# Optimization experiments

Measured on AMD Instinct MI355X. Metric: run time of the kernel, lower is better.

## Reference

```python
import jax, jax.numpy as jnp
import numpy as np

B, C, H, W = 16, 512, 64, 64
NH, HD = 8, 64  # num_heads, head_dim; C == NH*HD
EPS_ATTN = 1e-5
EPS_BN = 1e-5


def setup_inputs() -> dict:
    key = jax.random.key(0)
    k = jax.random.split(key, 9)
    x = jax.random.normal(k[0], (B, C, H, W), dtype=jnp.float32)
    # grouped 1x1 conv qkv: groups=NH, in/group=HD, out/group=3*HD
    w1 = jax.random.normal(k[1], (NH, 3 * HD, HD), dtype=jnp.float32) * 0.05
    b1 = jax.random.normal(k[2], (NH, 3 * HD), dtype=jnp.float32) * 0.01
    # grouped 1x1 conv qkv2: groups=HD, in/group=NH, out/group=3*NH
    w2 = jax.random.normal(k[3], (HD, 3 * NH, NH), dtype=jnp.float32) * 0.05
    b2 = jax.random.normal(k[4], (HD, 3 * NH), dtype=jnp.float32) * 0.01
    gamma = 1.0 + 0.1 * jax.random.normal(k[5], (C,), dtype=jnp.float32)
    beta = 0.1 * jax.random.normal(k[6], (C,), dtype=jnp.float32)
    rmean = 0.1 * jax.random.normal(k[7], (C,), dtype=jnp.float32)
    rvar = 0.5 + jax.random.uniform(k[8], (C,), dtype=jnp.float32)
    return {"x": x, "w1": w1, "b1": b1, "w2": w2, "b2": b2,
            "gamma": gamma, "beta": beta, "rmean": rmean, "rvar": rvar}


def _signed_sqrt_softmax(a):
    a = jnp.sign(a) * jnp.sqrt(jnp.abs(a) + EPS_ATTN)
    return jax.nn.softmax(a, axis=-1)


def reference(x, w1, b1, w2, b2, gamma, beta, rmean, rvar):
    N = H * W
    # ---- stage 1: grouped 1x1 conv (groups=NH) ----
    xg = x.reshape(B, NH, HD, N)
    qkv = jnp.einsum('goi,bgin->bgon', w1, xg) + b1[None, :, :, None]  # [B,NH,3HD,N]
    # torch grouped-conv channel order is group-major -> flatten then split as in source
    q, k, v = jnp.moveaxis(qkv.reshape(B, 3 * C, N).reshape(B, 3, NH, HD, N), 1, 0)
    attn = jnp.einsum('bhdn,bhen->bhde', q, k) * (HD ** -0.5)  # [B,NH,HD,HD]
    attn = _signed_sqrt_softmax(attn)
    out = jnp.einsum('bhde,bhen->bhdn', attn, v)  # [B,NH,HD,N]
    x1 = out.reshape(B, C, H, W) + x
    x1 = jnp.transpose(x1.reshape(B, NH, HD, H, W), (0, 2, 1, 3, 4)).reshape(B, C, H, W)
    # ---- BatchNorm2d (eval mode) + ReLU ----
    inv = gamma / jnp.sqrt(rvar + EPS_BN)
    y = x1 * inv[None, :, None, None] + (beta - rmean * inv)[None, :, None, None]
    xr = jnp.maximum(y, 0.0)
    # ---- stage 2: grouped 1x1 conv (groups=HD) ----
    xg2 = xr.reshape(B, HD, NH, N)
    qkv2 = jnp.einsum('goi,bgin->bgon', w2, xg2) + b2[None, :, :, None]  # [B,HD,3NH,N]
    q2, k2, v2 = jnp.moveaxis(qkv2.reshape(B, 3 * C, N).reshape(B, 3, HD, NH, N), 1, 0)
    attn2 = jnp.einsum('bdhn,bden->bdhe', q2, k2) * (NH ** -0.5)  # [B,HD,NH,NH]
    attn2 = _signed_sqrt_softmax(attn2)
    out2 = jnp.einsum('bdhe,bden->bdhn', attn2, v2)  # [B,HD,NH,N]
    x2 = jnp.transpose(out2.reshape(B, HD, NH, H, W), (0, 2, 1, 3, 4)).reshape(B, C, H, W) + y
    return x2
```

## Files before the change

kernel.cpp:

```cpp
#include <hip/hip_runtime.h>

#define N_ 4096

typedef __attribute__((ext_vector_type(8))) short bf16x8;
typedef __attribute__((ext_vector_type(4))) short bf16x4;
typedef __attribute__((ext_vector_type(4))) float f32x4;

__device__ __forceinline__ float ssqrt(float a) {
  if (a == 0.f) return 0.f;
  return copysignf(sqrtf(fabsf(a) + 1e-5f), a);
}

__device__ __forceinline__ ushort f2bf(float f) {
  uint u = __float_as_uint(f);
  u += 0x7fff + ((u >> 16) & 1);
  return (ushort)(u >> 16);
}
__device__ __forceinline__ float bf2f(ushort h) {
  return __uint_as_float((uint)h << 16);
}

__device__ __forceinline__ f32x4 mfma16(bf16x8 a, bf16x8 b, f32x4 c) {
  return __builtin_amdgcn_mfma_f32_16x16x32_bf16(a, b, c, 0, 0, 0);
}

__device__ __forceinline__ bf16x8 relu8(bf16x8 v) {
  union { bf16x8 h; uint u[4]; } x;
  x.h = v;
#pragma unroll
  for (int i = 0; i < 4; ++i) {
    uint m = x.u[i] & 0x80008000u;
    x.u[i] &= ~((m >> 15) * 0xFFFFu);
  }
  return x.h;
}

__device__ __forceinline__ bf16x8 ld8_b64(const ushort* p) {
  bf16x4 a = *(const bf16x4*)p;
  bf16x4 b = *(const bf16x4*)(p + 4);
  return (bf16x8){a[0], a[1], a[2], a[3], b[0], b[1], b[2], b[3]};
}

__global__ __launch_bounds__(256) void k1_gram(const float* __restrict__ x,
    float* __restrict__ Gp, float* __restrict__ sxq, float* __restrict__ sxk) {
  int bid = (blockIdx.x & 7) * 64 + (blockIdx.x >> 3);
  int s = bid >> 7, r = bid & 127;
  int b = r >> 3, h = r & 7;
  int gq = h / 3, gk = (8 + h) / 3;
  const float* A = x + ((size_t)b * 512 + gq * 64) * N_ + s * 1024;
  const float* B = x + ((size_t)b * 512 + gk * 64) * N_ + s * 1024;
  __shared__ __attribute__((aligned(16))) ushort Ah[64][72], Al[64][72];
  __shared__ __attribute__((aligned(16))) ushort Bh[64][72], Bl[64][72];
  int t = threadIdx.x;
  int lr = t >> 2, lq = t & 3;
  int l = t & 63, w = t >> 6;
  int mw = (w >> 1) * 32, nw = (w & 1) * 32;
  int fr = l & 15, ko = (l >> 4) * 8;
  float sumA = 0.f, sumB = 0.f;
  f32x4 acc[2][2];
#pragma unroll
  for (int i = 0; i < 2; ++i)
#pragma unroll
    for (int j = 0; j < 2; ++j) acc[i][j] = (f32x4){0.f, 0.f, 0.f, 0.f};

  for (int kt = 0; kt < 16; ++kt) {
    int kbase = kt * 64 + lq * 16;
#pragma unroll
    for (int j = 0; j < 4; ++j) {
      float4 va = *(const float4*)(A + (size_t)lr * N_ + kbase + j * 4);
      float4 vb = *(const float4*)(B + (size_t)lr * N_ + kbase + j * 4);
      sumA += va.x + va.y + va.z + va.w;
      sumB += vb.x + vb.y + vb.z + vb.w;
      ushort4 ha, la, hb, lb;
      ha.x = f2bf(va.x); ha.y = f2bf(va.y); ha.z = f2bf(va.z); ha.w = f2bf(va.w);
      la.x = f2bf(va.x - bf2f(ha.x)); la.y = f2bf(va.y - bf2f(ha.y));
      la.z = f2bf(va.z - bf2f(ha.z)); la.w = f2bf(va.w - bf2f(ha.w));
      hb.x = f2bf(vb.x); hb.y = f2bf(vb.y); hb.z = f2bf(vb.z); hb.w = f2bf(vb.w);
      lb.x = f2bf(vb.x - bf2f(hb.x)); lb.y = f2bf(vb.y - bf2f(hb.y));
      lb.z = f2bf(vb.z - bf2f(hb.z)); lb.w = f2bf(vb.w - bf2f(hb.w));
      int c0 = lq * 16 + j * 4;
      *(ushort4*)&Ah[lr][c0] = ha;
      *(ushort4*)&Al[lr][c0] = la;
      *(ushort4*)&Bh[lr][c0] = hb;
      *(ushort4*)&Bl[lr][c0] = lb;
    }
    __syncthreads();
#pragma unroll
    for (int wk = 0; wk < 2; ++wk) {
      int kk = wk * 32 + ko;
      bf16x8 ah[2], al[2], bh[2], bl[2];
#pragma unroll
      for (int mt = 0; mt < 2; ++mt) {
        ah[mt] = *(const bf16x8*)&Ah[mw + mt * 16 + fr][kk];
        al[mt] = *(const bf16x8*)&Al[mw + mt * 16 + fr][kk];
      }
#pragma unroll
      for (int nt = 0; nt < 2; ++nt) {
        bh[nt] = *(const bf16x8*)&Bh[nw + nt * 16 + fr][kk];
        bl[nt] = *(const bf16x8*)&Bl[nw + nt * 16 + fr][kk];
      }
#pragma unroll
      for (int mt = 0; mt < 2; ++mt)
#pragma unroll
        for (int nt = 0; nt < 2; ++nt) {
          acc[mt][nt] = mfma16(ah[mt], bh[nt], acc[mt][nt]);
          acc[mt][nt] = mfma16(ah[mt], bl[nt], acc[mt][nt]);
          acc[mt][nt] = mfma16(al[mt], bh[nt], acc[mt][nt]);
        }
    }
    __syncthreads();
  }
  size_t base = ((size_t)s * 128 + r) * 4096;
#pragma unroll
  for (int mt = 0; mt < 2; ++mt)
#pragma unroll
    for (int nt = 0; nt < 2; ++nt)
#pragma unroll
      for (int reg = 0; reg < 4; ++reg) {
        int gr = mw + mt * 16 + (l >> 4) * 4 + reg;
        int gc = nw + nt * 16 + fr;
        Gp[base + (size_t)gr * 64 + gc] = acc[mt][nt][reg];
      }
  sumA += __shfl_xor(sumA, 1); sumA += __shfl_xor(sumA, 2);
  sumB += __shfl_xor(sumB, 1); sumB += __shfl_xor(sumB, 2);
  if (lq == 0) {
    size_t sb = ((size_t)s * 128 + r) * 64;
    sxq[sb + lr] = sumA;
    sxk[sb + lr] = sumB;
  }
}

__global__ __launch_bounds__(256) void k2_attn1(
    const float* __restrict__ w1, const float* __restrict__ b1,
    const float* __restrict__ Gp, const float* __restrict__ sxqp,
    const float* __restrict__ sxkp,
    ushort* __restrict__ M1h, ushort* __restrict__ M1l,
    float* __restrict__ pbv1) {
  int bh = blockIdx.x;
  int h = bh & 7;
  int mq = h, mk = 8 + h, mv = 16 + h;
  int gq = mq / 3, oq0 = (mq % 3) * 64;
  int gk = mk / 3, ok0 = (mk % 3) * 64;
  int gv = mv / 3, ov0 = (mv % 3) * 64;
  __shared__ __attribute__((aligned(16))) float Gs[64][68];
  __shared__ __attribute__((aligned(16))) float Was[64][68];
  __shared__ __attribute__((aligned(16))) float Wbs[64][68];
  __shared__ __attribute__((aligned(16))) float Ts[64][68];
  __shared__ float sxs[64], sks[64], vqs[64], vks[64], bvs[64];
  int t = threadIdx.x, tx = t & 15, ty = t >> 4;
  int d0 = ty * 4, e0 = tx * 4;

  for (int f = t; f < 4096; f += 256) {
    int dd = f >> 6, ee = f & 63;
    float g = 0.f;
#pragma unroll
    for (int s = 0; s < 4; ++s) g += Gp[(((size_t)s * 128 + bh) * 64 + dd) * 64 + ee];
    Gs[dd][ee] = g;
    Was[dd][ee] = w1[((size_t)(gq * 192 + oq0 + dd)) * 64 + ee];
    Wbs[dd][ee] = w1[((size_t)(gk * 192 + ok0 + dd)) * 64 + ee];
  }
  if (t < 64) {
    float v = 0.f, w = 0.f;
#pragma unroll
    for (int s = 0; s < 4; ++s) {
      v += sxqp[((size_t)s * 128 + bh) * 64 + t];
      w += sxkp[((size_t)s * 128 + bh) * 64 + t];
    }
    sxs[t] = v; sks[t] = w;
    bvs[t] = b1[gv * 192 + ov0 + t];
  }
  __syncthreads();
  if (t < 64) {
    float vq = 0.f, vk = 0.f;
    for (int i = 0; i < 64; ++i) { vq += Was[t][i] * sxs[i]; vk += Wbs[t][i] * sks[i]; }
    vqs[t] = vq; vks[t] = vk;
  }
  {
    float acc[4][4] = {};
    for (int i = 0; i < 64; i += 4) {
      float4 a4[4], g4[4];
#pragma unroll
      for (int r = 0; r < 4; ++r) a4[r] = *(const float4*)&Was[d0 + r][i];
#pragma unroll
      for (int k = 0; k < 4; ++k) g4[k] = *(const float4*)&Gs[i + k][e0];
#pragma unroll
      for (int r = 0; r < 4; ++r) {
        const float* ap = (const float*)&a4[r];
#pragma unroll
        for (int k = 0; k < 4; ++k) {
          const float* gp = (const float*)&g4[k];
#pragma unroll
          for (int c = 0; c < 4; ++c) acc[r][c] += ap[k] * gp[c];
        }
      }
    }
#pragma unroll
    for (int r = 0; r < 4; ++r)
#pragma unroll
      for (int c = 0; c < 4; ++c) Ts[d0 + r][e0 + c] = acc[r][c];
  }
  __syncthreads();
  float P[4][4];
  {
    float s[4][4] = {};
    for (int j = 0; j < 64; j += 4) {
      float4 t4[4], w4[4];
#pragma unroll
      for (int r = 0; r < 4; ++r) t4[r] = *(const float4*)&Ts[d0 + r][j];
#pragma unroll
      for (int c = 0; c < 4; ++c) w4[c] = *(const float4*)&Wbs[e0 + c][j];
#pragma unroll
      for (int r = 0; r < 4; ++r)
#pragma unroll
        for (int c = 0; c < 4; ++c)
          s[r][c] += t4[r].x * w4[c].x + t4[r].y * w4[c].y
                   + t4[r].z * w4[c].z + t4[r].w * w4[c].w;
    }
    float bq_[4], bk_[4];
#pragma unroll
    for (int r = 0; r < 4; ++r) bq_[r] = b1[gq * 192 + oq0 + d0 + r];
#pragma unroll
    for (int c = 0; c < 4; ++c) bk_[c] = b1[gk * 192 + ok0 + e0 + c];
#pragma unroll
    for (int r = 0; r < 4; ++r)
#pragma unroll
      for (int c = 0; c < 4; ++c) {
        float v = (s[r][c] + bq_[r] * vks[e0 + c] + bk_[c] * vqs[d0 + r]
                   + 4096.f * bq_[r] * bk_[c]) * 0.125f;
        s[r][c] = ssqrt(v);
      }
#pragma unroll
    for (int r = 0; r < 4; ++r) {
      float m = fmaxf(fmaxf(s[r][0], s[r][1]), fmaxf(s[r][2], s[r][3]));
#pragma unroll
      for (int mm = 1; mm < 16; mm <<= 1) m = fmaxf(m, __shfl_xor(m, mm));
      float sum = 0.f;
#pragma unroll
      for (int c = 0; c < 4; ++c) { s[r][c] = expf(s[r][c] - m); sum += s[r][c]; }
#pragma unroll
      for (int mm = 1; mm < 16; mm <<= 1) sum += __shfl_xor(sum, mm);
      float inv = 1.f / sum;
#pragma unroll
      for (int c = 0; c < 4; ++c) P[r][c] = s[r][c] * inv;
    }
  }
#pragma unroll
  for (int r = 0; r < 4; ++r)
#pragma unroll
    for (int c = 0; c < 4; ++c) Gs[d0 + r][e0 + c] = P[r][c];
  for (int f = t; f < 4096; f += 256) {
    int ee = f >> 6, ii = f & 63;
    Was[ee][ii] = w1[((size_t)(gv * 192 + ov0 + ee)) * 64 + ii];
  }
  __syncthreads();
  {
    float acc[4][4] = {};
    for (int e = 0; e < 64; e += 4) {
      float4 p4[4], v4[4];
#pragma unroll
      for (int r = 0; r < 4; ++r) p4[r] = *(const float4*)&Gs[d0 + r][e];
#pragma unroll
      for (int k = 0; k < 4; ++k) v4[k] = *(const float4*)&Was[e + k][e0];
#pragma unroll
      for (int r = 0; r < 4; ++r) {
        const float* pp = (const float*)&p4[r];
#pragma unroll
        for (int k = 0; k < 4; ++k) {
          const float* vp = (const float*)&v4[k];
#pragma unroll
          for (int c = 0; c < 4; ++c) acc[r][c] += pp[k] * vp[c];
        }
      }
    }
    ushort* MoH = M1h + (size_t)bh * 4096;
    ushort* MoL = M1l + (size_t)bh * 4096;
#pragma unroll
    for (int r = 0; r < 4; ++r)
#pragma unroll
      for (int c = 0; c < 4; ++c) {
        float vv = acc[r][c];
        ushort hi = f2bf(vv);
        MoH[(size_t)(d0 + r) * 64 + e0 + c] = hi;
        MoL[(size_t)(d0 + r) * 64 + e0 + c] = f2bf(vv - bf2f(hi));
      }
  }
  if (t < 64) {
    float pb = 0.f;
    for (int e = 0; e < 64; ++e) pb += Gs[t][e] * bvs[e];
    pbv1[(size_t)bh * 64 + t] = pb;
  }
}

__global__ __launch_bounds__(256) void k3_out1(const float* __restrict__ x,
    const ushort* __restrict__ M1h, const ushort* __restrict__ M1l,
    const float* __restrict__ pbv1,
    const float* __restrict__ gamma, const float* __restrict__ beta,
    const float* __restrict__ rmean, const float* __restrict__ rvar,
    ushort* __restrict__ y) {
  int orig = (blockIdx.x & 7) * 256 + (blockIdx.x >> 3);
  int b = orig >> 7;
  int rem = orig & 127;
  int chunk = rem >> 3, h = rem & 7;
  int bh = b * 8 + h;
  int gv = (16 + h) / 3;
  const float* Xv = x + ((size_t)b * 512 + gv * 64) * N_ + chunk * 256;
  const float* Xr = x + ((size_t)b * 512 + h * 64) * N_ + chunk * 256;
  ushort* Y = y + (size_t)b * 512 * N_ + chunk * 256;

  __shared__ __attribute__((aligned(16))) ushort Xth[64][68], Xtl[64][68];
  __shared__ float pbs[64], invs[64], adds[64];
  int t = threadIdx.x;
  if (t < 64) {
    pbs[t] = pbv1[(size_t)bh * 64 + t];
    int c = t * 8 + h;
    float iv = gamma[c] / sqrtf(rvar[c] + 1e-5f);
    invs[t] = iv;
    adds[t] = beta[c] - rmean[c] * iv;
  }
  int l = t & 63, w = t >> 6;
  int dq = w >> 1, nq = w & 1;
  int fr = l & 15, g = l >> 4;

  bf16x8 mh[2][2], ml[2][2];
  {
    const ushort* MbH = M1h + (size_t)bh * 4096;
    const ushort* MbL = M1l + (size_t)bh * 4096;
#pragma unroll
    for (int dr = 0; dr < 2; ++dr)
#pragma unroll
      for (int wk = 0; wk < 2; ++wk) {
        int off = (dq * 32 + dr * 16 + fr) * 64 + wk * 32 + g * 8;
        mh[dr][wk] = *(const bf16x8*)(MbH + off);
        ml[dr][wk] = *(const bf16x8*)(MbL + off);
      }
  }

  int e2 = t >> 3, q = t & 7;
  for (int tile = 0; tile < 4; ++tile) {
    int nb = tile * 64;
    {
      const float* r0p = Xv + (size_t)(2 * e2) * N_ + nb + q * 8;
      const float* r1p = r0p + N_;
      float4 a0 = *(const float4*)r0p, a1 = *(const float4*)(r0p + 4);
      float4 b0 = *(const float4*)r1p, b1 = *(const float4*)(r1p + 4);
      float ra[8] = {a0.x, a0.y, a0.z, a0.w, a1.x, a1.y, a1.z, a1.w};
      float rb[8] = {b0.x, b0.y, b0.z, b0.w, b1.x, b1.y, b1.z, b1.w};
#pragma unroll
      for (int i = 0; i < 8; ++i) {
        int n = q * 8 + i;
        ushort h0 = f2bf(ra[i]), h1 = f2bf(rb[i]);
        ushort l0 = f2bf(ra[i] - bf2f(h0)), l1 = f2bf(rb[i] - bf2f(h1));
        *(uint*)&Xth[n][2 * e2] = (uint)h0 | ((uint)h1 << 16);
        *(uint*)&Xtl[n][2 * e2] = (uint)l0 | ((uint)l1 << 16);
      }
    }
    __syncthreads();
    f32x4 acc[2][2];
#pragma unroll
    for (int i = 0; i < 2; ++i)
#pragma unroll
      for (int j = 0; j < 2; ++j) acc[i][j] = (f32x4){0.f, 0.f, 0.f, 0.f};
#pragma unroll
    for (int wk = 0; wk < 2; ++wk) {
      int kk = wk * 32 + g * 8;
      bf16x8 xh[2], xl[2];
#pragma unroll
      for (int nr = 0; nr < 2; ++nr) {
        xh[nr] = ld8_b64(&Xth[nq * 32 + nr * 16 + fr][kk]);
        xl[nr] = ld8_b64(&Xtl[nq * 32 + nr * 16 + fr][kk]);
      }
#pragma unroll
      for (int nr = 0; nr < 2; ++nr)
#pragma unroll
        for (int dr = 0; dr < 2; ++dr) {
          acc[nr][dr] = mfma16(xh[nr], mh[dr][wk], acc[nr][dr]);
          acc[nr][dr] = mfma16(xh[nr], ml[dr][wk], acc[nr][dr]);
          acc[nr][dr] = mfma16(xl[nr], mh[dr][wk], acc[nr][dr]);
        }
    }
#pragma unroll
    for (int nr = 0; nr < 2; ++nr)
#pragma unroll
      for (int dr = 0; dr < 2; ++dr) {
        int d = dq * 32 + dr * 16 + fr;
        int n0 = nb + nq * 32 + nr * 16 + g * 4;
        float4 rx = *(const float4*)(Xr + (size_t)d * N_ + n0);
        float iv = invs[d], ad = adds[d], pb = pbs[d];
        float4 v;
        v.x = (acc[nr][dr][0] + pb + rx.x) * iv + ad;
        v.y = (acc[nr][dr][1] + pb + rx.y) * iv + ad;
        v.z = (acc[nr][dr][2] + pb + rx.z) * iv + ad;
        v.w = (acc[nr][dr][3] + pb + rx.w) * iv + ad;
        ushort4 o;
        o.x = f2bf(v.x); o.y = f2bf(v.y); o.z = f2bf(v.z); o.w = f2bf(v.w);
        *(ushort4*)(Y + (size_t)(d * 8 + h) * N_ + n0) = o;
      }
    __syncthreads();
  }
}

__global__ __launch_bounds__(256) void k46_stage2(const ushort* __restrict__ y,
    const float* __restrict__ w2, const float* __restrict__ b2,
    float* __restrict__ out) {
  int orig = (blockIdx.x & 7) * 128 + (blockIdx.x >> 3);
  int b = orig >> 6, d = orig & 63;
  int gq = d / 3, gk = (64 + d) / 3, gv = (128 + d) / 3;
  int mq = d, mk = 64 + d, mv = 128 + d;
  int g2q = mq / 3, oq0 = (mq % 3) * 8;
  int g2k = mk / 3, ok0 = (mk % 3) * 8;
  int g2v = mv / 3, ov0 = (mv % 3) * 8;
  const ushort* Aq = y + ((size_t)b * 512 + gq * 8) * N_;
  const ushort* Ak = y + ((size_t)b * 512 + gk * 8) * N_;
  int t = threadIdx.x;
  int l = t & 63, w = t >> 6;

  __shared__ float W2q[8][8], W2k[8][8], W2v[8][8];
  __shared__ float bq2[8], bk2[8], bv2[8];
  __shared__ float red[4][16][16];
  __shared__ float gbuf[80];
  __shared__ float Ps[8][9];
  __shared__ float Msh[8][8], pbsh[8];
  if (t < 64) {
    int hh = t >> 3, ee = t & 7;
    W2q[hh][ee] = w2[(size_t)(g2q * 24 + oq0 + hh) * 8 + ee];
    W2k[hh][ee] = w2[(size_t)(g2k * 24 + ok0 + hh) * 8 + ee];
    W2v[hh][ee] = w2[(size_t)(g2v * 24 + ov0 + hh) * 8 + ee];
  }
  if (t < 8) {
    bq2[t] = b2[g2q * 24 + oq0 + t];
    bk2[t] = b2[g2k * 24 + ok0 + t];
    bv2[t] = b2[g2v * 24 + ov0 + t];
  }

  {
    int row16 = l & 15;
    int ko = (l >> 4) * 8;
    const ushort* Arow = (row16 < 8) ? (Aq + (size_t)row16 * N_)
                                     : (Ak + (size_t)(row16 - 8) * N_);
    const ushort* Brow = (row16 < 8) ? (Ak + (size_t)row16 * N_) : nullptr;
    ushort bv = (row16 == 8) ? (ushort)0x3F80 : (ushort)0;
    bf16x8 bconst = {(short)bv, (short)bv, (short)bv, (short)bv,
                     (short)bv, (short)bv, (short)bv, (short)bv};
    f32x4 acc = (f32x4){0.f, 0.f, 0.f, 0.f};
    int nbase = w * 1024 + ko;
#pragma unroll 4
    for (int step = 0; step < 32; ++step) {
      int n0 = nbase + step * 32;
      bf16x8 a = relu8(*(const bf16x8*)(Arow + n0));
      bf16x8 bb;
      if (row16 < 8) bb = relu8(*(const bf16x8*)(Brow + n0));
      else bb = bconst;
      acc = mfma16(a, bb, acc);
    }
#pragma unroll
    for (int r = 0; r < 4; ++r) red[w][(l >> 4) * 4 + r][l & 15] = acc[r];
  }
  __syncthreads();
  {
    int rr = t >> 4, cc = t & 15;
    float csum = red[0][rr][cc] + red[1][rr][cc] + red[2][rr][cc] + red[3][rr][cc];
    if (rr < 8 && cc < 8) gbuf[rr * 8 + cc] = csum;
    else if (cc == 8) gbuf[rr < 8 ? 64 + rr : 72 + (rr - 8)] = csum;
  }
  __syncthreads();

  if (t < 64) {
    int hh = t >> 3, ee = t & 7;
    float s = 0.f;
#pragma unroll
    for (int i = 0; i < 8; ++i) {
      float pg = 0.f;
#pragma unroll
      for (int j = 0; j < 8; ++j) pg += gbuf[i * 8 + j] * W2k[ee][j];
      s += W2q[hh][i] * pg;
    }
    float dq = 0.f, dk = 0.f;
#pragma unroll
    for (int i = 0; i < 8; ++i) { dq += W2q[hh][i] * gbuf[64 + i]; dk += W2k[ee][i] * gbuf[72 + i]; }
    s = (s + bq2[hh] * dk + bk2[ee] * dq + 4096.f * bq2[hh] * bk2[ee]) * 0.35355339059327373f;
    s = ssqrt(s);
    float m = s;
#pragma unroll
    for (int mm = 1; mm < 8; mm <<= 1) m = fmaxf(m, __shfl_xor(m, mm));
    float p = expf(s - m);
    float sum = p;
#pragma unroll
    for (int mm = 1; mm < 8; mm <<= 1) sum += __shfl_xor(sum, mm);
    p /= sum;
    Ps[hh][ee] = p;
  }
  __syncthreads();
  if (t < 64) {
    int hh = t >> 3, ee = t & 7;
    float mo = 0.f;
#pragma unroll
    for (int e = 0; e < 8; ++e) mo += Ps[hh][e] * W2v[e][ee];
    Msh[hh][ee] = mo;
  }
  if (t < 8) {
    float pb = 0.f;
#pragma unroll
    for (int e = 0; e < 8; ++e) pb += Ps[t][e] * bv2[e];
    pbsh[t] = pb;
  }
  __syncthreads();

  float msr[8][8], pbr[8];
#pragma unroll
  for (int hh = 0; hh < 8; ++hh) {
    pbr[hh] = pbsh[hh];
#pragma unroll
    for (int i = 0; i < 8; ++i) msr[hh][i] = Msh[hh][i];
  }
  const ushort* Yv = y + ((size_t)b * 512 + gv * 8) * N_;
  const ushort* Yr = y + ((size_t)b * 512 + d) * N_;
  float* O = out + ((size_t)b * 512 + d) * N_;
  for (int it = 0; it < 4; ++it) {
    int n4 = (it * 256 + t) * 4;
    float xv0[8], xv1[8], xv2[8], xv3[8];
#pragma unroll
    for (int i = 0; i < 8; ++i) {
      ushort4 u = *(const ushort4*)(Yv + (size_t)i * N_ + n4);
      xv0[i] = fmaxf(bf2f(u.x), 0.f); xv1[i] = fmaxf(bf2f(u.y), 0.f);
      xv2[i] = fmaxf(bf2f(u.z), 0.f); xv3[i] = fmaxf(bf2f(u.w), 0.f);
    }
#pragma unroll
    for (int hh = 0; hh < 8; ++hh) {
      float4 a;
      a.x = pbr[hh]; a.y = pbr[hh]; a.z = pbr[hh]; a.w = pbr[hh];
#pragma unroll
      for (int i = 0; i < 8; ++i) {
        float m = msr[hh][i];
        a.x += m * xv0[i]; a.y += m * xv1[i];
        a.z += m * xv2[i]; a.w += m * xv3[i];
      }
      ushort4 r = *(const ushort4*)(Yr + (size_t)hh * 64 * N_ + n4);
      a.x += bf2f(r.x); a.y += bf2f(r.y); a.z += bf2f(r.z); a.w += bf2f(r.w);
      *(float4*)(O + (size_t)hh * 64 * N_ + n4) = a;
    }
  }
}

extern "C" void kernel_launch(void* const* d_in, const int* in_sizes, int n_in,
                              void* d_out, int out_size, void* d_ws, size_t ws_size,
                              hipStream_t stream) {
  const float* x     = (const float*)d_in[0];
  const float* w1    = (const float*)d_in[1];
  const float* b1    = (const float*)d_in[2];
  const float* w2    = (const float*)d_in[3];
  const float* b2    = (const float*)d_in[4];
  const float* gamma = (const float*)d_in[5];
  const float* beta  = (const float*)d_in[6];
  const float* rmean = (const float*)d_in[7];
  const float* rvar  = (const float*)d_in[8];
  float* out = (float*)d_out;

  ushort* y   = (ushort*)d_ws;
  float* Gp   = (float*)(y + 33554432);
  float* sxq  = Gp + 2097152;
  float* sxk  = sxq + 32768;
  ushort* M1h = (ushort*)(sxk + 32768);
  ushort* M1l = M1h + 524288;
  float* pbv1 = (float*)(M1l + 524288);
  size_t need = (size_t)67108864 + 8650752 + 2097152 + 32768;
  if (ws_size < need) return;

  k1_gram<<<512, 256, 0, stream>>>(x, Gp, sxq, sxk);
  k2_attn1<<<128, 256, 0, stream>>>(w1, b1, Gp, sxq, sxk, M1h, M1l, pbv1);
  k3_out1<<<2048, 256, 0, stream>>>(x, M1h, M1l, pbv1, gamma, beta, rmean, rvar, y);
  k46_stage2<<<1024, 256, 0, stream>>>(y, w2, b2, out);
}
```

Measured before the change: 176.4 us.

## Deduplicate gram blocks across heads sharing group pairs and use truncating bf16 split

The gram kernel previously computed one 64x64 Gram per head, but the 8 heads map onto only 6 distinct (q-group, k-group) pairs, so it now launches 384 blocks over the unique pairs and the attention kernel indexes them through a head-to-pair table. Row sums are stored per group instead of per head. The float-to-bf16 hi/lo split now truncates the high part instead of rounding, which saves ALU work in both the gram and output kernels. Truncation keeps the hi+lo sum accurate but changes how the error is distributed, and some row-sum writes are redundant when several pairs share a group.

```diff
diff --git a/kernel.cpp b/kernel.cpp
--- a/kernel.cpp
+++ b/kernel.cpp
@@ -20,6 +20,13 @@
   return __uint_as_float((uint)h << 16);
 }
 
+__device__ __forceinline__ void split2(float f, ushort& hi, ushort& lo) {
+  uint u = __float_as_uint(f);
+  hi = (ushort)(u >> 16);
+  float lof = f - __uint_as_float(u & 0xffff0000u);
+  lo = (ushort)(__float_as_uint(lof) >> 16);
+}
+
 __device__ __forceinline__ f32x4 mfma16(bf16x8 a, bf16x8 b, f32x4 c) {
   return __builtin_amdgcn_mfma_f32_16x16x32_bf16(a, b, c, 0, 0, 0);
 }
@@ -42,11 +49,13 @@
 }
 
 __global__ __launch_bounds__(256) void k1_gram(const float* __restrict__ x,
-    float* __restrict__ Gp, float* __restrict__ sxq, float* __restrict__ sxk) {
-  int bid = (blockIdx.x & 7) * 64 + (blockIdx.x >> 3);
-  int s = bid >> 7, r = bid & 127;
-  int b = r >> 3, h = r & 7;
-  int gq = h / 3, gk = (8 + h) / 3;
+    float* __restrict__ Gp, float* __restrict__ sums) {
+  const int GQ[6] = {0, 0, 1, 1, 2, 2};
+  const int GK[6] = {2, 3, 3, 4, 4, 5};
+  int bid = (blockIdx.x & 7) * 48 + (blockIdx.x >> 3);
+  int s = bid / 96, rem = bid % 96;
+  int b = rem / 6, pid = rem % 6;
+  int gq = GQ[pid], gk = GK[pid];
   const float* A = x + ((size_t)b * 512 + gq * 64) * N_ + s * 1024;
   const float* B = x + ((size_t)b * 512 + gk * 64) * N_ + s * 1024;
   __shared__ __attribute__((aligned(16))) ushort Ah[64][72], Al[64][72];
@@ -72,12 +81,10 @@
       sumA += va.x + va.y + va.z + va.w;
       sumB += vb.x + vb.y + vb.z + vb.w;
       ushort4 ha, la, hb, lb;
-      ha.x = f2bf(va.x); ha.y = f2bf(va.y); ha.z = f2bf(va.z); ha.w = f2bf(va.w);
-      la.x = f2bf(va.x - bf2f(ha.x)); la.y = f2bf(va.y - bf2f(ha.y));
-      la.z = f2bf(va.z - bf2f(ha.z)); la.w = f2bf(va.w - bf2f(ha.w));
-      hb.x = f2bf(vb.x); hb.y = f2bf(vb.y); hb.z = f2bf(vb.z); hb.w = f2bf(vb.w);
-      lb.x = f2bf(vb.x - bf2f(hb.x)); lb.y = f2bf(vb.y - bf2f(hb.y));
-      lb.z = f2bf(vb.z - bf2f(hb.z)); lb.w = f2bf(vb.w - bf2f(hb.w));
+      split2(va.x, ha.x, la.x); split2(va.y, ha.y, la.y);
+      split2(va.z, ha.z, la.z); split2(va.w, ha.w, la.w);
+      split2(vb.x, hb.x, lb.x); split2(vb.y, hb.y, lb.y);
+      split2(vb.z, hb.z, lb.z); split2(vb.w, hb.w, lb.w);
       int c0 = lq * 16 + j * 4;
       *(ushort4*)&Ah[lr][c0] = ha;
       *(ushort4*)&Al[lr][c0] = la;
@@ -110,7 +117,7 @@
     }
     __syncthreads();
   }
-  size_t base = ((size_t)s * 128 + r) * 4096;
+  size_t base = ((size_t)s * 96 + rem) * 4096;
 #pragma unroll
   for (int mt = 0; mt < 2; ++mt)
 #pragma unroll
@@ -124,20 +131,20 @@
   sumA += __shfl_xor(sumA, 1); sumA += __shfl_xor(sumA, 2);
   sumB += __shfl_xor(sumB, 1); sumB += __shfl_xor(sumB, 2);
   if (lq == 0) {
-    size_t sb = ((size_t)s * 128 + r) * 64;
-    sxq[sb + lr] = sumA;
-    sxk[sb + lr] = sumB;
+    sums[(((size_t)s * 16 + b) * 6 + gq) * 64 + lr] = sumA;
+    sums[(((size_t)s * 16 + b) * 6 + gk) * 64 + lr] = sumB;
   }
 }
 
 __global__ __launch_bounds__(256) void k2_attn1(
     const float* __restrict__ w1, const float* __restrict__ b1,
-    const float* __restrict__ Gp, const float* __restrict__ sxqp,
-    const float* __restrict__ sxkp,
+    const float* __restrict__ Gp, const float* __restrict__ sums,
     ushort* __restrict__ M1h, ushort* __restrict__ M1l,
     float* __restrict__ pbv1) {
+  const int PID[8] = {0, 1, 1, 2, 3, 3, 4, 5};
   int bh = blockIdx.x;
-  int h = bh & 7;
+  int b = bh >> 3, h = bh & 7;
+  int pid = PID[h];
   int mq = h, mk = 8 + h, mv = 16 + h;
   int gq = mq / 3, oq0 = (mq % 3) * 64;
   int gk = mk / 3, ok0 = (mk % 3) * 64;
@@ -154,7 +161,8 @@
     int dd = f >> 6, ee = f & 63;
     float g = 0.f;
 #pragma unroll
-    for (int s = 0; s < 4; ++s) g += Gp[(((size_t)s * 128 + bh) * 64 + dd) * 64 + ee];
+    for (int s = 0; s < 4; ++s)
+      g += Gp[((size_t)s * 96 + b * 6 + pid) * 4096 + f];
     Gs[dd][ee] = g;
     Was[dd][ee] = w1[((size_t)(gq * 192 + oq0 + dd)) * 64 + ee];
     Wbs[dd][ee] = w1[((size_t)(gk * 192 + ok0 + dd)) * 64 + ee];
@@ -163,8 +171,8 @@
     float v = 0.f, w = 0.f;
 #pragma unroll
     for (int s = 0; s < 4; ++s) {
-      v += sxqp[((size_t)s * 128 + bh) * 64 + t];
-      w += sxkp[((size_t)s * 128 + bh) * 64 + t];
+      v += sums[(((size_t)s * 16 + b) * 6 + gq) * 64 + t];
+      w += sums[(((size_t)s * 16 + b) * 6 + gk) * 64 + t];
     }
     sxs[t] = v; sks[t] = w;
     bvs[t] = b1[gv * 192 + ov0 + t];
@@ -348,8 +356,9 @@
 #pragma unroll
       for (int i = 0; i < 8; ++i) {
         int n = q * 8 + i;
-        ushort h0 = f2bf(ra[i]), h1 = f2bf(rb[i]);
-        ushort l0 = f2bf(ra[i] - bf2f(h0)), l1 = f2bf(rb[i] - bf2f(h1));
+        ushort h0, l0, h1, l1;
+        split2(ra[i], h0, l0);
+        split2(rb[i], h1, l1);
         *(uint*)&Xth[n][2 * e2] = (uint)h0 | ((uint)h1 << 16);
         *(uint*)&Xtl[n][2 * e2] = (uint)l0 | ((uint)l1 << 16);
       }
@@ -555,18 +564,17 @@
   const float* rvar  = (const float*)d_in[8];
   float* out = (float*)d_out;
 
-  ushort* y   = (ushort*)d_ws;
-  float* Gp   = (float*)(y + 33554432);
-  float* sxq  = Gp + 2097152;
-  float* sxk  = sxq + 32768;
-  ushort* M1h = (ushort*)(sxk + 32768);
-  ushort* M1l = M1h + 524288;
-  float* pbv1 = (float*)(M1l + 524288);
-  size_t need = (size_t)67108864 + 8650752 + 2097152 + 32768;
+  ushort* y    = (ushort*)d_ws;
+  float* Gp    = (float*)(y + 33554432);
+  float* sums  = Gp + 1572864;
+  ushort* M1h  = (ushort*)(sums + 24576);
+  ushort* M1l  = M1h + 524288;
+  float* pbv1  = (float*)(M1l + 524288);
+  size_t need = (size_t)67108864 + 6291456 + 98304 + 2097152 + 32768;
   if (ws_size < need) return;
 
-  k1_gram<<<512, 256, 0, stream>>>(x, Gp, sxq, sxk);
-  k2_attn1<<<128, 256, 0, stream>>>(w1, b1, Gp, sxq, sxk, M1h, M1l, pbv1);
+  k1_gram<<<384, 256, 0, stream>>>(x, Gp, sums);
+  k2_attn1<<<128, 256, 0, stream>>>(w1, b1, Gp, sums, M1h, M1l, pbv1);
   k3_out1<<<2048, 256, 0, stream>>>(x, M1h, M1l, pbv1, gamma, beta, rmean, rvar, y);
   k46_stage2<<<1024, 256, 0, stream>>>(y, w2, b2, out);
 }
```

Measured after the change: 169.2 us. 4.1% less time.
